# Kernel optimization log

Measured on AMD Instinct MI355X. Metric: run time of the kernel, lower is better.

The kernel has to match this reference:

```python
import jax, jax.numpy as jnp
import numpy as np

B, T, C = 4, 2048, 1024
N_HEADS = 16
HEAD_DIM = C // N_HEADS

def setup_inputs() -> dict:
    key = jax.random.key(0)
    k1, k2, k3 = jax.random.split(key, 3)
    x = jax.random.normal(k1, (B, T, C), dtype=jnp.float32)
    w_attn = jax.random.normal(k2, (C, 3 * C), dtype=jnp.float32) * (1.0 / np.sqrt(C))
    b_attn = jnp.zeros((3 * C,), dtype=jnp.float32)
    w_proj = jax.random.normal(k3, (C, C), dtype=jnp.float32) * (1.0 / np.sqrt(C))
    b_proj = jnp.zeros((C,), dtype=jnp.float32)
    return {"x": x, "w_attn": w_attn, "b_attn": b_attn, "w_proj": w_proj, "b_proj": b_proj}

def reference(x, w_attn, b_attn, w_proj, b_proj):
    Bx, Tx, Cx = x.shape
    qkv = x @ w_attn + b_attn                      # [B,T,3C]
    q, k, v = jnp.split(qkv, 3, axis=-1)
    def heads(t):
        return t.reshape(Bx, Tx, N_HEADS, HEAD_DIM).transpose(0, 2, 1, 3)  # [B,H,T,D]
    q, k, v = heads(q), heads(k), heads(v)
    scale = 1.0 / np.sqrt(HEAD_DIM)
    attn = jnp.einsum('bhqd,bhkd->bhqk', q, k) * scale  # [B,H,T,T]
    causal = jnp.tril(jnp.ones((Tx, Tx), dtype=bool))
    attn = jnp.where(causal[None, None, :, :], attn, -jnp.inf)
    attn = jax.nn.softmax(attn, axis=-1)
    out = jnp.einsum('bhqk,bhkd->bhqd', attn, v)        # [B,H,T,D]
    out = out.transpose(0, 2, 1, 3).reshape(Bx, Tx, Cx)
    return out @ w_proj + b_proj
```

## Files before the change

kernel.cpp:

```cpp
#include <hip/hip_runtime.h>
#include <hip/hip_bf16.h>

#define BATCH 4
#define SEQ   2048
#define CH    1024
#define NH    16
#define HD    64
#define BT    8192

typedef __attribute__((ext_vector_type(8))) short bf16x8;
typedef __attribute__((ext_vector_type(4))) float f32x4;
typedef __attribute__((ext_vector_type(16))) float f32x16;

__device__ __forceinline__ unsigned short f2b(float f) {
  __hip_bfloat16 h = __float2bfloat16(f);
  return *reinterpret_cast<unsigned short*>(&h);
}

__device__ __forceinline__ unsigned cvt_pk(float lo, float hi_) {
  unsigned r;
  asm("v_cvt_pk_bf16_f32 %0, %1, %2" : "=v"(r) : "v"(lo), "v"(hi_));
  return r;
}
__device__ __forceinline__ void plane_swap(unsigned &a, unsigned &b) {
  asm("v_permlane32_swap_b32 %0, %1" : "+v"(a), "+v"(b));
}


__global__ void conv_x_bf16(const float* __restrict__ in, unsigned short* __restrict__ out, int n4) {
  int i = blockIdx.x * blockDim.x + threadIdx.x;
  if (i >= n4) return;
  float4 v = reinterpret_cast<const float4*>(in)[i];
  ushort4 o;
  o.x = f2b(v.x); o.y = f2b(v.y); o.z = f2b(v.z); o.w = f2b(v.w);
  reinterpret_cast<ushort4*>(out)[i] = o;
}

__global__ void transpose_w_bf16(const float* __restrict__ in, unsigned short* __restrict__ out,
                                 int R, int Cc) {
  __shared__ float tile[32][33];
  int c0 = blockIdx.x * 32, r0 = blockIdx.y * 32;
  int tx = threadIdx.x, ty = threadIdx.y;
  #pragma unroll
  for (int i = 0; i < 32; i += 8)
    tile[ty + i][tx] = in[(size_t)(r0 + ty + i) * Cc + c0 + tx];
  __syncthreads();
  #pragma unroll
  for (int i = 0; i < 32; i += 8)
    out[(size_t)(c0 + ty + i) * R + r0 + tx] = f2b(tile[tx][ty + i]);
}


#define QSCALE 0.18033688011112042f

#define GSTAGE(BUF, K0)                                                                        \
  {                                                                                            \
    _Pragma("unroll")                                                                          \
    for (int c = 0; c < 2; ++c) {                                                              \
      int idx = c * 256 + tid;                                                                 \
      const unsigned short* sA = A + (size_t)(m0 + (idx >> 2)) * 1024 + (K0) + (idx & 3) * 8;  \
      __builtin_amdgcn_global_load_lds((const __attribute__((address_space(1))) void*)sA,      \
          (__attribute__((address_space(3))) void*)&sb[(BUF) * 4096 + (c * 256 + (tid & ~63)) * 8], 16, 0, 0); \
      const unsigned short* sB = Bt + (size_t)(n0 + (idx >> 2)) * 1024 + (K0) + (idx & 3) * 8; \
      __builtin_amdgcn_global_load_lds((const __attribute__((address_space(1))) void*)sB,      \
          (__attribute__((address_space(3))) void*)&sb[12288 + (BUF) * 4096 + (c * 256 + (tid & ~63)) * 8], 16, 0, 0); \
    }                                                                                          \
  }

__global__ __launch_bounds__(256) void gemm_qkv(
    const unsigned short* __restrict__ A,
    const unsigned short* __restrict__ Bt,
    const float* __restrict__ bias,
    unsigned short* __restrict__ Qb,
    unsigned short* __restrict__ Kb,
    unsigned short* __restrict__ Vt) {
  __shared__ __align__(16) unsigned short sb[24576];
  int tid = threadIdx.x;
  int lane = tid & 63, wav = tid >> 6;
  int wr = wav >> 1, wc = wav & 1;
  int lr = lane & 15, lh = lane >> 4;
  int m0 = blockIdx.x * 128, n0 = blockIdx.y * 128;

  f32x4 acc[4][4];
  #pragma unroll
  for (int i = 0; i < 4; ++i)
    #pragma unroll
    for (int j = 0; j < 4; ++j)
      acc[i][j] = f32x4{0.f, 0.f, 0.f, 0.f};

  GSTAGE(0, 0)
  GSTAGE(1, 32)
  asm volatile("s_waitcnt vmcnt(4)" ::: "memory");
  __builtin_amdgcn_s_barrier();

  int cur = 0;
  for (int k0 = 0; k0 < 1024; k0 += 32) {
    bool issued = (k0 + 64 < 1024);
    int nb = cur + 2; if (nb >= 3) nb -= 3;
    if (issued) GSTAGE(nb, k0 + 64)
    bf16x8 a[4], b[4];
    #pragma unroll
    for (int i = 0; i < 4; ++i)
      a[i] = *reinterpret_cast<const bf16x8*>(&sb[cur * 4096 + (wr * 64 + i * 16 + lr) * 32 + lh * 8]);
    #pragma unroll
    for (int j = 0; j < 4; ++j)
      b[j] = *reinterpret_cast<const bf16x8*>(&sb[12288 + cur * 4096 + (wc * 64 + j * 16 + lr) * 32 + lh * 8]);
    #pragma unroll
    for (int i = 0; i < 4; ++i)
      #pragma unroll
      for (int j = 0; j < 4; ++j)
        acc[i][j] = __builtin_amdgcn_mfma_f32_16x16x32_bf16(a[i], b[j], acc[i][j], 0, 0, 0);
    if (issued) { asm volatile("s_waitcnt vmcnt(4)" ::: "memory"); }
    else        { asm volatile("s_waitcnt vmcnt(0)" ::: "memory"); }
    __builtin_amdgcn_s_barrier();
    cur = (cur + 1 == 3) ? 0 : cur + 1;
  }

  int which = n0 >> 10;
  int h2 = (n0 >> 6) & 15;
  int bb = m0 >> 11, t0 = m0 & 2047;

  if (which < 2) {
    unsigned short* dst = which ? Kb : Qb;
    float sc = which ? 1.0f : QSCALE;
    size_t headbase = (size_t)(bb * 16 + h2 + wc) * SEQ;
    #pragma unroll
    for (int j = 0; j < 4; ++j) {
      int d = j * 16 + lr;
      float bv = bias[n0 + wc * 64 + d];
      #pragma unroll
      for (int i = 0; i < 4; ++i) {
        #pragma unroll
        for (int r = 0; r < 4; ++r) {
          int t = t0 + wr * 64 + i * 16 + lh * 4 + r;
          dst[(headbase + t) * HD + d] = f2b((acc[i][j][r] + bv) * sc);
        }
      }
    }
  } else {
    unsigned short* tile = sb;
    #pragma unroll
    for (int half = 0; half < 2; ++half) {
      if (wc == half) {
        #pragma unroll
        for (int j = 0; j < 4; ++j) {
          int nrow = j * 16 + lr;
          float bv = bias[n0 + half * 64 + nrow];
          int sw = nrow & 7;
          #pragma unroll
          for (int i = 0; i < 4; ++i) {
            int cm = wr * 16 + i * 4 + lh;
            unsigned lo = cvt_pk(acc[i][j][0] + bv, acc[i][j][1] + bv);
            unsigned hi_ = cvt_pk(acc[i][j][2] + bv, acc[i][j][3] + bv);
            unsigned long long val = (unsigned long long)lo | ((unsigned long long)hi_ << 32);
            *reinterpret_cast<unsigned long long*>(&tile[nrow * 128 + (cm ^ sw) * 4]) = val;
          }
        }
      }
      __syncthreads();
      size_t vbase = (size_t)((bb * 16 + h2 + half) * 64);
      #pragma unroll
      for (int it = 0; it < 4; ++it) {
        int pid = it * 256 + tid;
        int nrow = pid >> 4, p = pid & 15;
        int sw = nrow & 7;
        union { unsigned long long u[2]; bf16x8 v; } u;
        u.u[0] = *reinterpret_cast<const unsigned long long*>(&tile[nrow * 128 + ((2 * p) ^ sw) * 4]);
        u.u[1] = *reinterpret_cast<const unsigned long long*>(&tile[nrow * 128 + (((2 * p) ^ sw) ^ 1) * 4]);
        *reinterpret_cast<bf16x8*>(&Vt[(vbase + nrow) * SEQ + t0 + p * 8]) = u.v;
      }
      __syncthreads();
    }
  }
}


__global__ __launch_bounds__(512, 2) void attn_fwd(
    const unsigned short* __restrict__ Qb,
    const unsigned short* __restrict__ Kb,
    const unsigned short* __restrict__ Vt,
    unsigned short* __restrict__ AO) {
  __shared__ __align__(16) unsigned short sbuf[24576];

  int tid = threadIdx.x;
  int lane = tid & 63, w = tid >> 6;
  int ql = lane & 31, hi = lane >> 5;
  int bid = blockIdx.x;
  int head = bid & 63;
  int qs = 7 - (bid >> 6);
  int q0 = qs * 256;
  int nt = 4 * (qs + 1);
  int b = head >> 4, h = head & 15;

  const unsigned short* Qh = Qb + (size_t)head * SEQ * HD;
  const unsigned short* Kh = Kb + (size_t)head * SEQ * HD;
  const unsigned short* Vh = Vt + (size_t)head * HD * SEQ;

#define STAGE(BUF, KV0)                                                                        \
  {                                                                                            \
    int row_ = tid >> 3;                                                                       \
    int cg_ = (tid & 7) ^ (row_ & 7);                                                          \
    const unsigned short* srcK_ = Kh + (size_t)((KV0) + row_) * HD + cg_ * 8;                  \
    __builtin_amdgcn_global_load_lds((const __attribute__((address_space(1))) void*)srcK_,     \
        (__attribute__((address_space(3))) void*)&sbuf[(BUF) * 4096 + (tid & ~63) * 8], 16, 0, 0); \
    const unsigned short* srcV_ = Vh + (size_t)row_ * SEQ + (KV0) + cg_ * 8;                   \
    __builtin_amdgcn_global_load_lds((const __attribute__((address_space(1))) void*)srcV_,     \
        (__attribute__((address_space(3))) void*)&sbuf[12288 + (BUF) * 4096 + (tid & ~63) * 8], 16, 0, 0); \
  }

  int qg = q0 + w * 32 + ql;
  bf16x8 qf[4];
  #pragma unroll
  for (int dblk = 0; dblk < 4; ++dblk)
    qf[dblk] = *reinterpret_cast<const bf16x8*>(&Qh[(size_t)qg * HD + dblk * 16 + hi * 8]);

  f32x16 o0 = (f32x16)0.0f, o1 = (f32x16)0.0f;
  float mrun = -1e30f, lrun = 0.f;

  STAGE(0, 0)
  STAGE(1, 64)
  asm volatile("s_waitcnt vmcnt(2)" ::: "memory");
  __builtin_amdgcn_s_barrier();

  int cur = 0;
  int wq_hi = q0 + w * 32 + 31;
  for (int t = 0; t < nt; ++t) {
    int kv0 = t * 64;
    bool issued = (t + 2 < nt);
    int nb = cur + 2; if (nb >= 3) nb -= 3;
    if (issued) STAGE(nb, kv0 + 128)

    if (kv0 <= wq_hi) {
      f32x16 s0 = (f32x16)0.0f, s1 = (f32x16)0.0f;
      int rk0 = ql, rk1 = 32 + ql;
      __builtin_amdgcn_s_setprio(1);
      #pragma unroll
      for (int dblk = 0; dblk < 4; ++dblk) {
        bf16x8 kf0 = *reinterpret_cast<const bf16x8*>(
            &sbuf[cur * 4096 + rk0 * 64 + (((dblk * 2 + hi) ^ (rk0 & 7)) << 3)]);
        s0 = __builtin_amdgcn_mfma_f32_32x32x16_bf16(kf0, qf[dblk], s0, 0, 0, 0);
        bf16x8 kf1 = *reinterpret_cast<const bf16x8*>(
            &sbuf[cur * 4096 + rk1 * 64 + (((dblk * 2 + hi) ^ (rk1 & 7)) << 3)]);
        s1 = __builtin_amdgcn_mfma_f32_32x32x16_bf16(kf1, qf[dblk], s1, 0, 0, 0);
      }
      __builtin_amdgcn_s_setprio(0);

      float p[32];
      bool needMask = (kv0 + 63 > q0 + 32 * w);
      #pragma unroll
      for (int r = 0; r < 16; ++r) {
        int cr = (r & 3) + 8 * (r >> 2);
        float v0 = s0[r], v1 = s1[r];
        if (needMask) {
          int kv_ = kv0 + 4 * hi + cr;
          v0 = (kv_ > qg) ? -1e30f : v0;
          v1 = (kv_ + 32 > qg) ? -1e30f : v1;
        }
        p[r] = v0; p[16 + r] = v1;
      }

      float m16[16], m8[8], m4[4], m2[2];
      #pragma unroll
      for (int i = 0; i < 16; ++i) m16[i] = fmaxf(p[i], p[i + 16]);
      #pragma unroll
      for (int i = 0; i < 8; ++i) m8[i] = fmaxf(m16[i], m16[i + 8]);
      #pragma unroll
      for (int i = 0; i < 4; ++i) m4[i] = fmaxf(m8[i], m8[i + 4]);
      m2[0] = fmaxf(m4[0], m4[2]); m2[1] = fmaxf(m4[1], m4[3]);
      float mt = fmaxf(m2[0], m2[1]);
      mt = fmaxf(mt, __shfl_xor(mt, 32));
      float mnew = fmaxf(mrun, mt);
      float alpha = __builtin_amdgcn_exp2f(mrun - mnew);
      mrun = mnew;

      #pragma unroll
      for (int i = 0; i < 32; ++i) p[i] = __builtin_amdgcn_exp2f(p[i] - mnew);
      float a16[16], a8[8], a4[4];
      #pragma unroll
      for (int i = 0; i < 16; ++i) a16[i] = p[i] + p[i + 16];
      #pragma unroll
      for (int i = 0; i < 8; ++i) a8[i] = a16[i] + a16[i + 8];
      #pragma unroll
      for (int i = 0; i < 4; ++i) a4[i] = a8[i] + a8[i + 4];
      float rs = (a4[0] + a4[1]) + (a4[2] + a4[3]);
      rs += __shfl_xor(rs, 32);
      lrun = lrun * alpha + rs;

      #pragma unroll
      for (int i = 0; i < 16; ++i) { o0[i] *= alpha; o1[i] *= alpha; }

      union FU { unsigned u[4]; bf16x8 v; };
      FU fr[4];
      #pragma unroll
      for (int blk = 0; blk < 2; ++blk) {
        unsigned X = cvt_pk(p[blk * 16 + 0], p[blk * 16 + 1]);
        unsigned Z = cvt_pk(p[blk * 16 + 4], p[blk * 16 + 5]);
        plane_swap(X, Z);
        unsigned Y = cvt_pk(p[blk * 16 + 2], p[blk * 16 + 3]);
        unsigned W = cvt_pk(p[blk * 16 + 6], p[blk * 16 + 7]);
        plane_swap(Y, W);
        fr[blk * 2].u[0] = X; fr[blk * 2].u[1] = Y; fr[blk * 2].u[2] = Z; fr[blk * 2].u[3] = W;
        unsigned X2 = cvt_pk(p[blk * 16 + 8], p[blk * 16 + 9]);
        unsigned Z2 = cvt_pk(p[blk * 16 + 12], p[blk * 16 + 13]);
        plane_swap(X2, Z2);
        unsigned Y2 = cvt_pk(p[blk * 16 + 10], p[blk * 16 + 11]);
        unsigned W2 = cvt_pk(p[blk * 16 + 14], p[blk * 16 + 15]);
        plane_swap(Y2, W2);
        fr[blk * 2 + 1].u[0] = X2; fr[blk * 2 + 1].u[1] = Y2;
        fr[blk * 2 + 1].u[2] = Z2; fr[blk * 2 + 1].u[3] = W2;
      }

      __builtin_amdgcn_s_setprio(1);
      #pragma unroll
      for (int kc = 0; kc < 4; ++kc) {
        int rd0 = ql, rd1 = 32 + ql;
        bf16x8 vf0 = *reinterpret_cast<const bf16x8*>(
            &sbuf[12288 + cur * 4096 + rd0 * 64 + ((((kc << 1) + hi) ^ (rd0 & 7)) << 3)]);
        o0 = __builtin_amdgcn_mfma_f32_32x32x16_bf16(vf0, fr[kc].v, o0, 0, 0, 0);
        bf16x8 vf1 = *reinterpret_cast<const bf16x8*>(
            &sbuf[12288 + cur * 4096 + rd1 * 64 + ((((kc << 1) + hi) ^ (rd1 & 7)) << 3)]);
        o1 = __builtin_amdgcn_mfma_f32_32x32x16_bf16(vf1, fr[kc].v, o1, 0, 0, 0);
      }
      __builtin_amdgcn_s_setprio(0);
    }

    if (issued) { asm volatile("s_waitcnt vmcnt(2)" ::: "memory"); }
    else        { asm volatile("s_waitcnt vmcnt(0)" ::: "memory"); }
    __builtin_amdgcn_s_barrier();
    cur = (cur + 1 == 3) ? 0 : cur + 1;
  }

  float inv = 1.0f / lrun;
  int qloc = w * 32 + ql;
  #pragma unroll
  for (int dblk = 0; dblk < 2; ++dblk) {
    #pragma unroll
    for (int m = 0; m < 4; ++m) {
      float v0, v1, v2, v3;
      if (dblk == 0) {
        v0 = o0[m * 4 + 0] * inv; v1 = o0[m * 4 + 1] * inv;
        v2 = o0[m * 4 + 2] * inv; v3 = o0[m * 4 + 3] * inv;
      } else {
        v0 = o1[m * 4 + 0] * inv; v1 = o1[m * 4 + 1] * inv;
        v2 = o1[m * 4 + 2] * inv; v3 = o1[m * 4 + 3] * inv;
      }
      unsigned u0 = (unsigned)f2b(v0) | ((unsigned)f2b(v1) << 16);
      unsigned u1 = (unsigned)f2b(v2) | ((unsigned)f2b(v3) << 16);
      int slot = (dblk * 4 + m) ^ (qloc & 7);
      unsigned long long val = (unsigned long long)u0 | ((unsigned long long)u1 << 32);
      *reinterpret_cast<unsigned long long*>(&sbuf[qloc * 64 + slot * 8 + hi * 4]) = val;
    }
  }
  __syncthreads();

  #pragma unroll
  for (int it = 0; it < 4; ++it) {
    int qr = it * 64 + (tid >> 3);
    int lc = tid & 7;
    int slot = lc ^ (qr & 7);
    bf16x8 v = *reinterpret_cast<const bf16x8*>(&sbuf[qr * 64 + slot * 8]);
    *reinterpret_cast<bf16x8*>(
        &AO[(size_t)(b * SEQ + q0 + qr) * CH + h * 64 + lc * 8]) = v;
  }
}


__global__ __launch_bounds__(256) void gemm_proj(
    const unsigned short* __restrict__ A,
    const unsigned short* __restrict__ Bt,
    const float* __restrict__ bias,
    float* __restrict__ out) {
  __shared__ __align__(16) unsigned short sb[24576];
  int tid = threadIdx.x;
  int lane = tid & 63, wav = tid >> 6;
  int wr = wav >> 1, wc = wav & 1;
  int lr = lane & 15, lh = lane >> 4;
  int m0 = blockIdx.x * 128, n0 = blockIdx.y * 128;

  f32x4 acc[4][4];
  #pragma unroll
  for (int i = 0; i < 4; ++i)
    #pragma unroll
    for (int j = 0; j < 4; ++j)
      acc[i][j] = f32x4{0.f, 0.f, 0.f, 0.f};

  GSTAGE(0, 0)
  GSTAGE(1, 32)
  asm volatile("s_waitcnt vmcnt(4)" ::: "memory");
  __builtin_amdgcn_s_barrier();

  int cur = 0;
  for (int k0 = 0; k0 < 1024; k0 += 32) {
    bool issued = (k0 + 64 < 1024);
    int nb = cur + 2; if (nb >= 3) nb -= 3;
    if (issued) GSTAGE(nb, k0 + 64)
    bf16x8 a[4], b[4];
    #pragma unroll
    for (int i = 0; i < 4; ++i)
      a[i] = *reinterpret_cast<const bf16x8*>(&sb[cur * 4096 + (wr * 64 + i * 16 + lr) * 32 + lh * 8]);
    #pragma unroll
    for (int j = 0; j < 4; ++j)
      b[j] = *reinterpret_cast<const bf16x8*>(&sb[12288 + cur * 4096 + (wc * 64 + j * 16 + lr) * 32 + lh * 8]);
    #pragma unroll
    for (int i = 0; i < 4; ++i)
      #pragma unroll
      for (int j = 0; j < 4; ++j)
        acc[i][j] = __builtin_amdgcn_mfma_f32_16x16x32_bf16(a[i], b[j], acc[i][j], 0, 0, 0);
    if (issued) { asm volatile("s_waitcnt vmcnt(4)" ::: "memory"); }
    else        { asm volatile("s_waitcnt vmcnt(0)" ::: "memory"); }
    __builtin_amdgcn_s_barrier();
    cur = (cur + 1 == 3) ? 0 : cur + 1;
  }

  #pragma unroll
  for (int i = 0; i < 4; ++i) {
    #pragma unroll
    for (int j = 0; j < 4; ++j) {
      int n = n0 + wc * 64 + j * 16 + lr;
      float bv = bias[n];
      #pragma unroll
      for (int r = 0; r < 4; ++r) {
        int m = m0 + wr * 64 + i * 16 + lh * 4 + r;
        out[(size_t)m * 1024 + n] = acc[i][j][r] + bv;
      }
    }
  }
}


extern "C" void kernel_launch(void* const* d_in, const int* in_sizes, int n_in,
                              void* d_out, int out_size, void* d_ws, size_t ws_size,
                              hipStream_t stream) {
  const float* x      = (const float*)d_in[0];
  const float* w_attn = (const float*)d_in[1];
  const float* b_attn = (const float*)d_in[2];
  const float* w_proj = (const float*)d_in[3];
  const float* b_proj = (const float*)d_in[4];
  float* out = (float*)d_out;

  char* ws = (char*)d_ws;
  unsigned short* xb  = (unsigned short*)(ws);
  unsigned short* wAT = (unsigned short*)(ws + 16777216);
  unsigned short* wPT = (unsigned short*)(ws + 23068672);
  unsigned short* Qb  = (unsigned short*)(ws + 25165824);
  unsigned short* Kb  = (unsigned short*)(ws + 41943040);
  unsigned short* Vt  = (unsigned short*)(ws + 58720256);
  unsigned short* AO  = (unsigned short*)(ws + 75497472);

  conv_x_bf16<<<(BT * CH / 4 + 255) / 256, 256, 0, stream>>>(x, xb, BT * CH / 4);
  transpose_w_bf16<<<dim3(3 * CH / 32, CH / 32), dim3(32, 8), 0, stream>>>(w_attn, wAT, CH, 3 * CH);
  transpose_w_bf16<<<dim3(CH / 32, CH / 32), dim3(32, 8), 0, stream>>>(w_proj, wPT, CH, CH);
  gemm_qkv<<<dim3(BT / 128, 3 * CH / 128), 256, 0, stream>>>(xb, wAT, b_attn, Qb, Kb, Vt);
  attn_fwd<<<512, 512, 0, stream>>>(Qb, Kb, Vt, AO);
  gemm_proj<<<dim3(BT / 128, CH / 128), 256, 0, stream>>>(AO, wPT, b_proj, out);
}
```

Baseline: 170.9 us.

## Switch attention KV pipeline to double-buffered 128-row tiles

The attention kernel now stages 128 KV rows per step into two buffers instead of 64-row tiles across a triple buffer, with a 16-chunk XOR swizzle for the V tile. Each outer iteration processes two 64-row sub-tiles between barriers, halving the number of barriers and wait points. LDS use grows to 64 KB per block, and prefetch depth drops from two tiles ahead to one, with a full vmcnt(0) wait each step.

```diff
diff --git a/kernel.cpp b/kernel.cpp
--- a/kernel.cpp
+++ b/kernel.cpp
@@ -180,7 +180,7 @@
     const unsigned short* __restrict__ Kb,
     const unsigned short* __restrict__ Vt,
     unsigned short* __restrict__ AO) {
-  __shared__ __align__(16) unsigned short sbuf[24576];
+  __shared__ __align__(16) unsigned short sbuf[32768];
 
   int tid = threadIdx.x;
   int lane = tid & 63, w = tid >> 6;
@@ -189,23 +189,29 @@
   int head = bid & 63;
   int qs = 7 - (bid >> 6);
   int q0 = qs * 256;
-  int nt = 4 * (qs + 1);
+  int NT = 2 * (qs + 1);
   int b = head >> 4, h = head & 15;
 
   const unsigned short* Qh = Qb + (size_t)head * SEQ * HD;
   const unsigned short* Kh = Kb + (size_t)head * SEQ * HD;
   const unsigned short* Vh = Vt + (size_t)head * HD * SEQ;
 
-#define STAGE(BUF, KV0)                                                                        \
+#define STAGE128(BUF, KV0)                                                                     \
   {                                                                                            \
-    int row_ = tid >> 3;                                                                       \
-    int cg_ = (tid & 7) ^ (row_ & 7);                                                          \
-    const unsigned short* srcK_ = Kh + (size_t)((KV0) + row_) * HD + cg_ * 8;                  \
-    __builtin_amdgcn_global_load_lds((const __attribute__((address_space(1))) void*)srcK_,     \
-        (__attribute__((address_space(3))) void*)&sbuf[(BUF) * 4096 + (tid & ~63) * 8], 16, 0, 0); \
-    const unsigned short* srcV_ = Vh + (size_t)row_ * SEQ + (KV0) + cg_ * 8;                   \
-    __builtin_amdgcn_global_load_lds((const __attribute__((address_space(1))) void*)srcV_,     \
-        (__attribute__((address_space(3))) void*)&sbuf[12288 + (BUF) * 4096 + (tid & ~63) * 8], 16, 0, 0); \
+    _Pragma("unroll")                                                                          \
+    for (int c = 0; c < 2; ++c) {                                                              \
+      int idx = c * 512 + tid;                                                                 \
+      int krow = idx >> 3;                                                                     \
+      int kcg = (idx & 7) ^ (krow & 7);                                                        \
+      const unsigned short* srcK_ = Kh + (size_t)((KV0) + krow) * HD + kcg * 8;                \
+      __builtin_amdgcn_global_load_lds((const __attribute__((address_space(1))) void*)srcK_,   \
+          (__attribute__((address_space(3))) void*)&sbuf[(BUF) * 8192 + (c * 512 + (tid & ~63)) * 8], 16, 0, 0); \
+      int vrow = idx >> 4;                                                                     \
+      int vcg = (idx & 15) ^ (vrow & 15);                                                      \
+      const unsigned short* srcV_ = Vh + (size_t)vrow * SEQ + (KV0) + vcg * 8;                 \
+      __builtin_amdgcn_global_load_lds((const __attribute__((address_space(1))) void*)srcV_,   \
+          (__attribute__((address_space(3))) void*)&sbuf[16384 + (BUF) * 8192 + (c * 512 + (tid & ~63)) * 8], 16, 0, 0); \
+    }                                                                                          \
   }
 
   int qg = q0 + w * 32 + ql;
@@ -217,117 +223,118 @@
   f32x16 o0 = (f32x16)0.0f, o1 = (f32x16)0.0f;
   float mrun = -1e30f, lrun = 0.f;
 
-  STAGE(0, 0)
-  STAGE(1, 64)
-  asm volatile("s_waitcnt vmcnt(2)" ::: "memory");
+  STAGE128(0, 0)
+  asm volatile("s_waitcnt vmcnt(0)" ::: "memory");
   __builtin_amdgcn_s_barrier();
 
   int cur = 0;
   int wq_hi = q0 + w * 32 + 31;
-  for (int t = 0; t < nt; ++t) {
-    int kv0 = t * 64;
-    bool issued = (t + 2 < nt);
-    int nb = cur + 2; if (nb >= 3) nb -= 3;
-    if (issued) STAGE(nb, kv0 + 128)
-
-    if (kv0 <= wq_hi) {
-      f32x16 s0 = (f32x16)0.0f, s1 = (f32x16)0.0f;
-      int rk0 = ql, rk1 = 32 + ql;
-      __builtin_amdgcn_s_setprio(1);
-      #pragma unroll
-      for (int dblk = 0; dblk < 4; ++dblk) {
-        bf16x8 kf0 = *reinterpret_cast<const bf16x8*>(
-            &sbuf[cur * 4096 + rk0 * 64 + (((dblk * 2 + hi) ^ (rk0 & 7)) << 3)]);
-        s0 = __builtin_amdgcn_mfma_f32_32x32x16_bf16(kf0, qf[dblk], s0, 0, 0, 0);
-        bf16x8 kf1 = *reinterpret_cast<const bf16x8*>(
-            &sbuf[cur * 4096 + rk1 * 64 + (((dblk * 2 + hi) ^ (rk1 & 7)) << 3)]);
-        s1 = __builtin_amdgcn_mfma_f32_32x32x16_bf16(kf1, qf[dblk], s1, 0, 0, 0);
-      }
-      __builtin_amdgcn_s_setprio(0);
-
-      float p[32];
-      bool needMask = (kv0 + 63 > q0 + 32 * w);
-      #pragma unroll
-      for (int r = 0; r < 16; ++r) {
-        int cr = (r & 3) + 8 * (r >> 2);
-        float v0 = s0[r], v1 = s1[r];
-        if (needMask) {
-          int kv_ = kv0 + 4 * hi + cr;
-          v0 = (kv_ > qg) ? -1e30f : v0;
-          v1 = (kv_ + 32 > qg) ? -1e30f : v1;
-        }
-        p[r] = v0; p[16 + r] = v1;
-      }
-
-      float m16[16], m8[8], m4[4], m2[2];
-      #pragma unroll
-      for (int i = 0; i < 16; ++i) m16[i] = fmaxf(p[i], p[i + 16]);
-      #pragma unroll
-      for (int i = 0; i < 8; ++i) m8[i] = fmaxf(m16[i], m16[i + 8]);
-      #pragma unroll
-      for (int i = 0; i < 4; ++i) m4[i] = fmaxf(m8[i], m8[i + 4]);
-      m2[0] = fmaxf(m4[0], m4[2]); m2[1] = fmaxf(m4[1], m4[3]);
-      float mt = fmaxf(m2[0], m2[1]);
-      mt = fmaxf(mt, __shfl_xor(mt, 32));
-      float mnew = fmaxf(mrun, mt);
-      float alpha = __builtin_amdgcn_exp2f(mrun - mnew);
-      mrun = mnew;
-
-      #pragma unroll
-      for (int i = 0; i < 32; ++i) p[i] = __builtin_amdgcn_exp2f(p[i] - mnew);
-      float a16[16], a8[8], a4[4];
-      #pragma unroll
-      for (int i = 0; i < 16; ++i) a16[i] = p[i] + p[i + 16];
-      #pragma unroll
-      for (int i = 0; i < 8; ++i) a8[i] = a16[i] + a16[i + 8];
-      #pragma unroll
-      for (int i = 0; i < 4; ++i) a4[i] = a8[i] + a8[i + 4];
-      float rs = (a4[0] + a4[1]) + (a4[2] + a4[3]);
-      rs += __shfl_xor(rs, 32);
-      lrun = lrun * alpha + rs;
-
-      #pragma unroll
-      for (int i = 0; i < 16; ++i) { o0[i] *= alpha; o1[i] *= alpha; }
-
-      union FU { unsigned u[4]; bf16x8 v; };
-      FU fr[4];
-      #pragma unroll
-      for (int blk = 0; blk < 2; ++blk) {
-        unsigned X = cvt_pk(p[blk * 16 + 0], p[blk * 16 + 1]);
-        unsigned Z = cvt_pk(p[blk * 16 + 4], p[blk * 16 + 5]);
-        plane_swap(X, Z);
-        unsigned Y = cvt_pk(p[blk * 16 + 2], p[blk * 16 + 3]);
-        unsigned W = cvt_pk(p[blk * 16 + 6], p[blk * 16 + 7]);
-        plane_swap(Y, W);
-        fr[blk * 2].u[0] = X; fr[blk * 2].u[1] = Y; fr[blk * 2].u[2] = Z; fr[blk * 2].u[3] = W;
-        unsigned X2 = cvt_pk(p[blk * 16 + 8], p[blk * 16 + 9]);
-        unsigned Z2 = cvt_pk(p[blk * 16 + 12], p[blk * 16 + 13]);
-        plane_swap(X2, Z2);
-        unsigned Y2 = cvt_pk(p[blk * 16 + 10], p[blk * 16 + 11]);
-        unsigned W2 = cvt_pk(p[blk * 16 + 14], p[blk * 16 + 15]);
-        plane_swap(Y2, W2);
-        fr[blk * 2 + 1].u[0] = X2; fr[blk * 2 + 1].u[1] = Y2;
-        fr[blk * 2 + 1].u[2] = Z2; fr[blk * 2 + 1].u[3] = W2;
-      }
-
-      __builtin_amdgcn_s_setprio(1);
-      #pragma unroll
-      for (int kc = 0; kc < 4; ++kc) {
-        int rd0 = ql, rd1 = 32 + ql;
-        bf16x8 vf0 = *reinterpret_cast<const bf16x8*>(
-            &sbuf[12288 + cur * 4096 + rd0 * 64 + ((((kc << 1) + hi) ^ (rd0 & 7)) << 3)]);
-        o0 = __builtin_amdgcn_mfma_f32_32x32x16_bf16(vf0, fr[kc].v, o0, 0, 0, 0);
-        bf16x8 vf1 = *reinterpret_cast<const bf16x8*>(
-            &sbuf[12288 + cur * 4096 + rd1 * 64 + ((((kc << 1) + hi) ^ (rd1 & 7)) << 3)]);
-        o1 = __builtin_amdgcn_mfma_f32_32x32x16_bf16(vf1, fr[kc].v, o1, 0, 0, 0);
-      }
-      __builtin_amdgcn_s_setprio(0);
+  for (int t = 0; t < NT; ++t) {
+    int tkv0 = t * 128;
+    if (t + 1 < NT) STAGE128(cur ^ 1, tkv0 + 128)
+
+    #pragma unroll
+    for (int sub = 0; sub < 2; ++sub) {
+      int kv0 = tkv0 + sub * 64;
+      if (kv0 <= wq_hi) {
+        f32x16 s0 = (f32x16)0.0f, s1 = (f32x16)0.0f;
+        int rk0 = sub * 64 + ql, rk1 = sub * 64 + 32 + ql;
+        __builtin_amdgcn_s_setprio(1);
+        #pragma unroll
+        for (int dblk = 0; dblk < 4; ++dblk) {
+          bf16x8 kf0 = *reinterpret_cast<const bf16x8*>(
+              &sbuf[cur * 8192 + rk0 * 64 + (((dblk * 2 + hi) ^ (rk0 & 7)) << 3)]);
+          s0 = __builtin_amdgcn_mfma_f32_32x32x16_bf16(kf0, qf[dblk], s0, 0, 0, 0);
+          bf16x8 kf1 = *reinterpret_cast<const bf16x8*>(
+              &sbuf[cur * 8192 + rk1 * 64 + (((dblk * 2 + hi) ^ (rk1 & 7)) << 3)]);
+          s1 = __builtin_amdgcn_mfma_f32_32x32x16_bf16(kf1, qf[dblk], s1, 0, 0, 0);
+        }
+        __builtin_amdgcn_s_setprio(0);
+
+        float p[32];
+        bool needMask = (kv0 + 63 > q0 + 32 * w);
+        #pragma unroll
+        for (int r = 0; r < 16; ++r) {
+          int cr = (r & 3) + 8 * (r >> 2);
+          float v0 = s0[r], v1 = s1[r];
+          if (needMask) {
+            int kv_ = kv0 + 4 * hi + cr;
+            v0 = (kv_ > qg) ? -1e30f : v0;
+            v1 = (kv_ + 32 > qg) ? -1e30f : v1;
+          }
+          p[r] = v0; p[16 + r] = v1;
+        }
+
+        float m16[16], m8[8], m4[4], m2[2];
+        #pragma unroll
+        for (int i = 0; i < 16; ++i) m16[i] = fmaxf(p[i], p[i + 16]);
+        #pragma unroll
+        for (int i = 0; i < 8; ++i) m8[i] = fmaxf(m16[i], m16[i + 8]);
+        #pragma unroll
+        for (int i = 0; i < 4; ++i) m4[i] = fmaxf(m8[i], m8[i + 4]);
+        m2[0] = fmaxf(m4[0], m4[2]); m2[1] = fmaxf(m4[1], m4[3]);
+        float mt = fmaxf(m2[0], m2[1]);
+        mt = fmaxf(mt, __shfl_xor(mt, 32));
+        float mnew = fmaxf(mrun, mt);
+        float alpha = __builtin_amdgcn_exp2f(mrun - mnew);
+        mrun = mnew;
+
+        #pragma unroll
+        for (int i = 0; i < 32; ++i) p[i] = __builtin_amdgcn_exp2f(p[i] - mnew);
+        float a16[16], a8[8], a4[4];
+        #pragma unroll
+        for (int i = 0; i < 16; ++i) a16[i] = p[i] + p[i + 16];
+        #pragma unroll
+        for (int i = 0; i < 8; ++i) a8[i] = a16[i] + a16[i + 8];
+        #pragma unroll
+        for (int i = 0; i < 4; ++i) a4[i] = a8[i] + a8[i + 4];
+        float rs = (a4[0] + a4[1]) + (a4[2] + a4[3]);
+        rs += __shfl_xor(rs, 32);
+        lrun = lrun * alpha + rs;
+
+        #pragma unroll
+        for (int i = 0; i < 16; ++i) { o0[i] *= alpha; o1[i] *= alpha; }
+
+        union FU { unsigned u[4]; bf16x8 v; };
+        FU fr[4];
+        #pragma unroll
+        for (int blk = 0; blk < 2; ++blk) {
+          unsigned X = cvt_pk(p[blk * 16 + 0], p[blk * 16 + 1]);
+          unsigned Z = cvt_pk(p[blk * 16 + 4], p[blk * 16 + 5]);
+          plane_swap(X, Z);
+          unsigned Y = cvt_pk(p[blk * 16 + 2], p[blk * 16 + 3]);
+          unsigned W = cvt_pk(p[blk * 16 + 6], p[blk * 16 + 7]);
+          plane_swap(Y, W);
+          fr[blk * 2].u[0] = X; fr[blk * 2].u[1] = Y; fr[blk * 2].u[2] = Z; fr[blk * 2].u[3] = W;
+          unsigned X2 = cvt_pk(p[blk * 16 + 8], p[blk * 16 + 9]);
+          unsigned Z2 = cvt_pk(p[blk * 16 + 12], p[blk * 16 + 13]);
+          plane_swap(X2, Z2);
+          unsigned Y2 = cvt_pk(p[blk * 16 + 10], p[blk * 16 + 11]);
+          unsigned W2 = cvt_pk(p[blk * 16 + 14], p[blk * 16 + 15]);
+          plane_swap(Y2, W2);
+          fr[blk * 2 + 1].u[0] = X2; fr[blk * 2 + 1].u[1] = Y2;
+          fr[blk * 2 + 1].u[2] = Z2; fr[blk * 2 + 1].u[3] = W2;
+        }
+
+        __builtin_amdgcn_s_setprio(1);
+        #pragma unroll
+        for (int kc = 0; kc < 4; ++kc) {
+          int rd0 = ql, rd1 = 32 + ql;
+          int gch = sub * 8 + (kc << 1) + hi;
+          bf16x8 vf0 = *reinterpret_cast<const bf16x8*>(
+              &sbuf[16384 + cur * 8192 + rd0 * 128 + ((gch ^ (rd0 & 15)) << 3)]);
+          o0 = __builtin_amdgcn_mfma_f32_32x32x16_bf16(vf0, fr[kc].v, o0, 0, 0, 0);
+          bf16x8 vf1 = *reinterpret_cast<const bf16x8*>(
+              &sbuf[16384 + cur * 8192 + rd1 * 128 + ((gch ^ (rd1 & 15)) << 3)]);
+          o1 = __builtin_amdgcn_mfma_f32_32x32x16_bf16(vf1, fr[kc].v, o1, 0, 0, 0);
+        }
+        __builtin_amdgcn_s_setprio(0);
+      }
     }
 
-    if (issued) { asm volatile("s_waitcnt vmcnt(2)" ::: "memory"); }
-    else        { asm volatile("s_waitcnt vmcnt(0)" ::: "memory"); }
+    asm volatile("s_waitcnt vmcnt(0)" ::: "memory");
     __builtin_amdgcn_s_barrier();
-    cur = (cur + 1 == 3) ? 0 : cur + 1;
+    cur ^= 1;
   }
 
   float inv = 1.0f / lrun;
```

After: 164.7 us. 1.04x faster.
